# Performance work log

Hardware: AMD Instinct MI355X
Metric: run time of the kernel (lower is better)

## Reference

```python
import jax, jax.numpy as jnp
import numpy as np

N = 100000   # nodes
E = 1200000  # edges
D = 64       # dim == num_features
L = 5        # num_gc_layers
G = 128      # num graphs in batch
BN_EPS = 1e-5
NORM_EPS = 1e-12

def setup_inputs() -> dict:
    key = jax.random.key(0)
    ks = jax.random.split(key, 16)
    s = 0.05
    x = jax.random.normal(ks[0], (N, D), jnp.float32)
    edge_index = jax.random.randint(ks[1], (2, E), 0, N, dtype=jnp.int32)
    batch = jnp.sort(jax.random.randint(ks[2], (N,), 0, G, dtype=jnp.int32))
    # Encoder_support: Linear(D, D)
    Ws = jax.random.normal(ks[3], (D, D), jnp.float32) * s
    bs = jnp.zeros((D,), jnp.float32)
    # GIN MLPs per layer: Linear(D,D) -> ReLU -> Linear(D,D)
    W1 = jax.random.normal(ks[4], (L, D, D), jnp.float32) * s
    b1 = jnp.zeros((L, D), jnp.float32)
    W2 = jax.random.normal(ks[5], (L, D, D), jnp.float32) * s
    b2 = jnp.zeros((L, D), jnp.float32)
    # BatchNorm affine params
    bn_gamma = jnp.ones((L, D), jnp.float32)
    bn_beta = jnp.zeros((L, D), jnp.float32)
    # proj_head: Linear(L*D, L*D) -> ReLU -> Linear(L*D, L*D)
    Wp1 = jax.random.normal(ks[6], (L * D, L * D), jnp.float32) * s
    bp1 = jnp.zeros((L * D,), jnp.float32)
    Wp2 = jax.random.normal(ks[7], (L * D, L * D), jnp.float32) * s
    bp2 = jnp.zeros((L * D,), jnp.float32)
    return {"x": x, "edge_index": edge_index, "batch": batch,
            "Ws": Ws, "bs": bs, "W1": W1, "b1": b1, "W2": W2, "b2": b2,
            "bn_gamma": bn_gamma, "bn_beta": bn_beta,
            "Wp1": Wp1, "bp1": bp1, "Wp2": Wp2, "bp2": bp2}

def _l2norm(v):
    # F.normalize(v, dim=1): v / max(||v||_2, 1e-12)
    n = jnp.sqrt(jnp.sum(v * v, axis=1, keepdims=True))
    return v / jnp.maximum(n, NORM_EPS)

def reference(x, edge_index, batch, Ws, bs, W1, b1, W2, b2,
              bn_gamma, bn_beta, Wp1, bp1, Wp2, bp2):
    src, dst = edge_index[0], edge_index[1]
    h = x @ Ws + bs  # Encoder_support
    xs = []
    for i in range(L):
        # GINConv (eps=0): nn(x + sum_{j->i} x_j)
        agg = jax.ops.segment_sum(h[src], dst, num_segments=N)  # [N, D]
        z = h + agg
        z = jnp.maximum(z @ W1[i] + b1[i], 0.0) @ W2[i] + b2[i]
        z = jnp.maximum(z, 0.0)  # F.relu after conv
        # BatchNorm1d (training-mode batch stats over nodes)
        mean = jnp.mean(z, axis=0)
        var = jnp.var(z, axis=0)
        h = bn_gamma[i] * (z - mean) * jax.lax.rsqrt(var + BN_EPS) + bn_beta[i]
        xs.append(h)
    # global_add_pool per layer, concat along feature dim -> [G, L*D]
    pooled = jnp.concatenate(
        [jax.ops.segment_sum(h_, batch, num_segments=G) for h_ in xs], axis=1)
    y = jnp.maximum(pooled @ Wp1 + bp1, 0.0) @ Wp2 + bp2
    return (_l2norm(y), _l2norm(pooled))
```

## Files before the change

kernel.cpp:

```cpp
#include <hip/hip_runtime.h>
#include <hip/hip_bf16.h>
#include <hip/hip_fp16.h>

constexpr int Nn = 100000;
constexpr int Ee = 1200000;
constexpr int Ll = 5;
constexpr int Gg = 128;
constexpr int PDim = 320;
constexpr int GG = (Nn + 63) / 64;

constexpr int NB    = 98;
constexpr int BCAP  = 16384;
constexpr int CHUNK = 4096;
constexpr int NBLK_A = (Ee + CHUNK - 1) / CHUNK;

typedef float f32x4 __attribute__((ext_vector_type(4)));
typedef _Float16 half8 __attribute__((ext_vector_type(8)));

union U4H8 { uint4 u; half8 h; };

__device__ inline ushort f2h(float f) {
    const __half h = __float2half(f);
    return *(const ushort*)&h;
}
__device__ inline uint pack2h(float lo, float hi) {
    return (uint)f2h(lo) | ((uint)f2h(hi) << 16);
}
__device__ inline float h2f_lo(uint u) {
    const ushort s = (ushort)(u & 0xffffu);
    return __half2float(*(const __half*)&s);
}
__device__ inline float h2f_hi(uint u) {
    const ushort s = (ushort)(u >> 16);
    return __half2float(*(const __half*)&s);
}

__device__ inline int lower_bound_i(const int* __restrict__ a, int n, int v)
{
    int lo = 0, hi = n;
    while (lo < hi) {
        const int m = (lo + hi) >> 1;
        if (a[m] < v) lo = m + 1; else hi = m;
    }
    return lo;
}

__global__ void init_csr(const int* __restrict__ batch, int* __restrict__ gCursor,
                         int* __restrict__ cnt, float* __restrict__ sc)
{
    const int t = threadIdx.x;
    if (t < NB) gCursor[t] = t * BCAP;
    {
        const int lo = lower_bound_i(batch, Nn, t);
        const int hi = lower_bound_i(batch, Nn, t + 1);
        cnt[t] = hi - lo;
    }
    if (t < 64) { sc[t] = 1.f; sc[64 + t] = 0.f; }
}

__global__ __launch_bounds__(256) void conv_weights(
    const float* __restrict__ Ws, const float* __restrict__ W1,
    const float* __restrict__ W2, ushort* __restrict__ WThi,
    ushort* __restrict__ WTlo)
{
    const int m = blockIdx.x;
    const float* src = (m == 0) ? Ws
                     : (m <= 5) ? W1 + (size_t)(m - 1) * 4096
                                : W2 + (size_t)(m - 6) * 4096;
    ushort* dh = WThi + (size_t)m * 4096;
    ushort* dl = WTlo + (size_t)m * 4096;
    const int t = threadIdx.x;
    const int col = t & 63;
    const int k0 = (t >> 6) * 16;
    #pragma unroll
    for (int i = 0; i < 16; i++) {
        const int k = k0 + i;
        const float w = src[k * 64 + col];
        const ushort h = f2h(w);
        dh[col * 64 + k] = h;
        const float resid = (w - h2f_lo((uint)h)) * 2048.0f;
        dl[col * 64 + k] = f2h(resid);
    }
}

__global__ __launch_bounds__(256) void gemm_enc(
    const float* __restrict__ A1,
    const ushort* __restrict__ WThi, const ushort* __restrict__ WTlo,
    const float* __restrict__ bias, ushort* __restrict__ Ys)
{
    const int t = threadIdx.x;
    const int w = t >> 6;
    const int l = t & 63;
    const int lr = l & 15;
    const int lk = l >> 4;

    half8 bHi[4][2], bLo[4][2];
    #pragma unroll
    for (int nt = 0; nt < 4; nt++)
        #pragma unroll
        for (int c = 0; c < 2; c++) {
            const int off = (nt * 16 + lr) * 64 + c * 32 + lk * 8;
            U4H8 uh, ul;
            uh.u = *(const uint4*)(WThi + off);
            ul.u = *(const uint4*)(WTlo + off);
            bHi[nt][c] = uh.h;
            bLo[nt][c] = ul.h;
        }

    const int arow = blockIdx.x * 64 + w * 16 + lr;
    half8 aHi[2], aLo[2];
    if (arow < Nn) {
        #pragma unroll
        for (int c = 0; c < 2; c++) {
            const float* p1 = A1 + (size_t)arow * 64 + c * 32 + lk * 8;
            U4H8 rh, rl;
            #pragma unroll
            for (int i = 0; i < 8; i++) {
                const float xv = p1[i];
                const _Float16 xh = (_Float16)xv;
                rh.h[i] = xh;
                rl.h[i] = (_Float16)((xv - (float)xh) * 2048.0f);
            }
            aHi[c] = rh.h;
            aLo[c] = rl.h;
        }
    } else {
        U4H8 z; z.u = make_uint4(0, 0, 0, 0);
        aHi[0] = aHi[1] = z.h;
        aLo[0] = aLo[1] = z.h;
    }

    f32x4 accH[4] = {}, accL[4] = {};
    #pragma unroll
    for (int nt = 0; nt < 4; nt++)
        #pragma unroll
        for (int c = 0; c < 2; c++) {
            accH[nt] = __builtin_amdgcn_mfma_f32_16x16x32_f16(
                aHi[c], bHi[nt][c], accH[nt], 0, 0, 0);
            accL[nt] = __builtin_amdgcn_mfma_f32_16x16x32_f16(
                aHi[c], bLo[nt][c], accL[nt], 0, 0, 0);
            accL[nt] = __builtin_amdgcn_mfma_f32_16x16x32_f16(
                aLo[c], bHi[nt][c], accL[nt], 0, 0, 0);
        }

    #pragma unroll
    for (int nt = 0; nt < 4; nt++) {
        const int ccol = nt * 16 + lr;
        const float bb = bias[ccol];
        #pragma unroll
        for (int j = 0; j < 4; j++) {
            const int crow = blockIdx.x * 64 + w * 16 + lk * 4 + j;
            if (crow < Nn)
                Ys[(size_t)crow * 64 + ccol] =
                    f2h(fmaf(accL[nt][j], 1.0f / 2048.0f, accH[nt][j]) + bb);
        }
    }
}

__global__ __launch_bounds__(256) void fused_mlp(
    const ushort* __restrict__ Us,
    const ushort* __restrict__ WT1hi, const ushort* __restrict__ WT1lo,
    const float* __restrict__ b1v,
    const ushort* __restrict__ WT2hi, const ushort* __restrict__ WT2lo,
    const float* __restrict__ b2v,
    ushort* __restrict__ Zs, float* __restrict__ spart)
{
    const int t = threadIdx.x;
    const int w = t >> 6;
    const int l = t & 63;
    const int lr = l & 15;
    const int lk = l >> 4;

    __shared__ ushort Mh[64][72];
    __shared__ float red[2][4][4][16];

    half8 b1Hi[4][2], b1Lo[4][2];
    #pragma unroll
    for (int nt = 0; nt < 4; nt++)
        #pragma unroll
        for (int c = 0; c < 2; c++) {
            const int off = (nt * 16 + lr) * 64 + c * 32 + lk * 8;
            U4H8 uh, ul;
            uh.u = *(const uint4*)(WT1hi + off);
            ul.u = *(const uint4*)(WT1lo + off);
            b1Hi[nt][c] = uh.h;
            b1Lo[nt][c] = ul.h;
        }

    const int arow = blockIdx.x * 64 + w * 16 + lr;
    half8 aF[2];
    if (arow < Nn) {
        U4H8 v0, v1;
        v0.u = *(const uint4*)(Us + (size_t)arow * 64 + lk * 8);
        v1.u = *(const uint4*)(Us + (size_t)arow * 64 + 32 + lk * 8);
        aF[0] = v0.h;
        aF[1] = v1.h;
    } else {
        U4H8 z; z.u = make_uint4(0, 0, 0, 0);
        aF[0] = aF[1] = z.h;
    }

    f32x4 accH[4] = {}, accL[4] = {};
    #pragma unroll
    for (int nt = 0; nt < 4; nt++)
        #pragma unroll
        for (int c = 0; c < 2; c++) {
            accH[nt] = __builtin_amdgcn_mfma_f32_16x16x32_f16(
                aF[c], b1Hi[nt][c], accH[nt], 0, 0, 0);
            accL[nt] = __builtin_amdgcn_mfma_f32_16x16x32_f16(
                aF[c], b1Lo[nt][c], accL[nt], 0, 0, 0);
        }

    #pragma unroll
    for (int nt = 0; nt < 4; nt++) {
        const int ccol = nt * 16 + lr;
        const float bb = b1v[ccol];
        #pragma unroll
        for (int j = 0; j < 4; j++) {
            const int rloc = w * 16 + lk * 4 + j;
            const float m = fmaxf(fmaf(accL[nt][j], 1.0f / 2048.0f, accH[nt][j]) + bb, 0.f);
            Mh[rloc][ccol] = f2h(m);
        }
    }
    __syncthreads();

    half8 b2Hi[4][2], b2Lo[4][2];
    #pragma unroll
    for (int nt = 0; nt < 4; nt++)
        #pragma unroll
        for (int c = 0; c < 2; c++) {
            const int off = (nt * 16 + lr) * 64 + c * 32 + lk * 8;
            U4H8 uh, ul;
            uh.u = *(const uint4*)(WT2hi + off);
            ul.u = *(const uint4*)(WT2lo + off);
            b2Hi[nt][c] = uh.h;
            b2Lo[nt][c] = ul.h;
        }

    half8 a2F[2];
    #pragma unroll
    for (int c = 0; c < 2; c++) {
        U4H8 v;
        v.u = *(const uint4*)&Mh[w * 16 + lr][c * 32 + lk * 8];
        a2F[c] = v.h;
    }

    f32x4 acc2H[4] = {}, acc2L[4] = {};
    #pragma unroll
    for (int nt = 0; nt < 4; nt++)
        #pragma unroll
        for (int c = 0; c < 2; c++) {
            acc2H[nt] = __builtin_amdgcn_mfma_f32_16x16x32_f16(
                a2F[c], b2Hi[nt][c], acc2H[nt], 0, 0, 0);
            acc2L[nt] = __builtin_amdgcn_mfma_f32_16x16x32_f16(
                a2F[c], b2Lo[nt][c], acc2L[nt], 0, 0, 0);
        }

    float s[4], s2[4];
    #pragma unroll
    for (int nt = 0; nt < 4; nt++) {
        const int ccol = nt * 16 + lr;
        const float bb = b2v[ccol];
        s[nt] = 0.f; s2[nt] = 0.f;
        #pragma unroll
        for (int j = 0; j < 4; j++) {
            const int crow = blockIdx.x * 64 + w * 16 + lk * 4 + j;
            if (crow < Nn) {
                const float v = fmaxf(fmaf(acc2L[nt][j], 1.0f / 2048.0f, acc2H[nt][j]) + bb, 0.f);
                Zs[(size_t)crow * 64 + ccol] = f2h(v);
                s[nt] += v; s2[nt] += v * v;
            }
        }
    }

    #pragma unroll
    for (int nt = 0; nt < 4; nt++) {
        s[nt]  += __shfl_xor(s[nt], 16);  s[nt]  += __shfl_xor(s[nt], 32);
        s2[nt] += __shfl_xor(s2[nt], 16); s2[nt] += __shfl_xor(s2[nt], 32);
    }
    if (l < 16) {
        #pragma unroll
        for (int nt = 0; nt < 4; nt++) {
            red[0][w][nt][l] = s[nt];
            red[1][w][nt][l] = s2[nt];
        }
    }
    __syncthreads();
    if (t < 64) {
        float ts = 0.f, ts2 = 0.f;
        #pragma unroll
        for (int wv = 0; wv < 4; wv++) {
            ts  += red[0][wv][t >> 4][t & 15];
            ts2 += red[1][wv][t >> 4][t & 15];
        }
        spart[(size_t)blockIdx.x * 128 + t] = ts;
        spart[(size_t)blockIdx.x * 128 + 64 + t] = ts2;
    }
}

__global__ __launch_bounds__(256) void reduce_stats(
    const float* __restrict__ spart, float* __restrict__ stats)
{
    const int t = threadIdx.x;
    const int col = t & 127;
    const int half = t >> 7;
    const int r0 = blockIdx.x * 98;
    const int r1 = min(r0 + 98, GG);
    float acc = 0.f;
    for (int r = r0 + half; r < r1; r += 2)
        acc += spart[(size_t)r * 128 + col];
    atomicAdd(&stats[col], acc);
}

__global__ __launch_bounds__(256) void bin_edges(
    const int* __restrict__ ei, int* __restrict__ gCursor,
    uint2* __restrict__ binned)
{
    __shared__ int hist[NB];
    __shared__ int base[NB];
    __shared__ int cur[NB];
    const int t = threadIdx.x;
    const int e0 = blockIdx.x * CHUNK;
    const int eEnd = min(e0 + CHUNK, Ee);
    if (t < NB) hist[t] = 0;
    __syncthreads();
    for (int e = e0 + t; e < eEnd; e += 256)
        atomicAdd(&hist[ei[Ee + e] >> 10], 1);
    __syncthreads();
    if (t < NB) {
        base[t] = atomicAdd(&gCursor[t], hist[t]);
        cur[t] = 0;
    }
    __syncthreads();
    for (int e = e0 + t; e < eEnd; e += 256) {
        const int s = ei[e];
        const int d = ei[Ee + e];
        const int b = d >> 10;
        const int pos = atomicAdd(&cur[b], 1);
        binned[(size_t)base[b] + pos] = make_uint2((uint)d, (uint)s);
    }
}

__global__ __launch_bounds__(128) void scan_buckets(
    const int* __restrict__ gCursor, int* __restrict__ bucketBase)
{
    __shared__ int sh[128];
    const int t = threadIdx.x;
    const int c = (t < NB) ? gCursor[t] - t * BCAP : 0;
    sh[t] = c;
    __syncthreads();
    for (int off = 1; off < 128; off <<= 1) {
        const int u = (t >= off) ? sh[t - off] : 0;
        __syncthreads();
        sh[t] += u;
        __syncthreads();
    }
    bucketBase[t] = sh[t] - c;
}

__global__ __launch_bounds__(256) void build_csr(
    const uint2* __restrict__ binned, const int* __restrict__ gCursor,
    const int* __restrict__ bucketBase, int* __restrict__ rowptr,
    int* __restrict__ colidx)
{
    __shared__ int degS[1024];
    __shared__ int sh[256];
    __shared__ int colStage[BCAP];
    const int b = blockIdx.x;
    const int t = threadIdx.x;
    const int cnt = gCursor[b] - b * BCAP;
    const int base = bucketBase[b];
    const uint2* src = binned + (size_t)b * BCAP;

    for (int i = t; i < 1024; i += 256) degS[i] = 0;
    __syncthreads();
    for (int i = t; i < cnt; i += 256)
        atomicAdd(&degS[src[i].x & 1023], 1);
    __syncthreads();

    const int b4 = t * 4;
    const int v0 = degS[b4], v1 = degS[b4 + 1], v2 = degS[b4 + 2], v3 = degS[b4 + 3];
    const int sSum = v0 + v1 + v2 + v3;
    sh[t] = sSum;
    __syncthreads();
    for (int off = 1; off < 256; off <<= 1) {
        const int u = (t >= off) ? sh[t - off] : 0;
        __syncthreads();
        sh[t] += u;
        __syncthreads();
    }
    const int excl = sh[t] - sSum;
    const int p0 = excl, p1 = excl + v0, p2 = excl + v0 + v1, p3 = excl + v0 + v1 + v2;

    const int grow = b * 1024 + b4;
    if (grow + 3 <= Nn) {
        *(int4*)(rowptr + grow) = make_int4(base + p0, base + p1, base + p2, base + p3);
    } else {
        if (grow + 0 <= Nn) rowptr[grow + 0] = base + p0;
        if (grow + 1 <= Nn) rowptr[grow + 1] = base + p1;
        if (grow + 2 <= Nn) rowptr[grow + 2] = base + p2;
        if (grow + 3 <= Nn) rowptr[grow + 3] = base + p3;
    }

    degS[b4] = p0; degS[b4 + 1] = p1; degS[b4 + 2] = p2; degS[b4 + 3] = p3;
    __syncthreads();
    for (int i = t; i < cnt; i += 256) {
        const uint2 p = src[i];
        const int pos = atomicAdd(&degS[p.x & 1023], 1);
        colStage[pos] = (int)p.y;
    }
    __syncthreads();
    for (int i = t; i < cnt; i += 256) colidx[base + i] = colStage[i];
}

__global__ __launch_bounds__(256) void gather_bn(
    const int* __restrict__ rowptr, const int* __restrict__ col,
    const ushort* __restrict__ zs, const float* __restrict__ sc,
    ushort* __restrict__ us)
{
    __shared__ float scS[128];
    const int t = threadIdx.x;
    if (t < 128) scS[t] = sc[t];
    __syncthreads();

    const int r = blockIdx.x * 32 + (t >> 3);
    const int q = t & 7;
    const int beg = rowptr[r], end = rowptr[r + 1];
    float a[8];
    {
        const uint4 v = *(const uint4*)(zs + (size_t)r * 64 + q * 8);
        a[0] = h2f_lo(v.x); a[1] = h2f_hi(v.x);
        a[2] = h2f_lo(v.y); a[3] = h2f_hi(v.y);
        a[4] = h2f_lo(v.z); a[5] = h2f_hi(v.z);
        a[6] = h2f_lo(v.w); a[7] = h2f_hi(v.w);
    }
    int j = beg;
    const int end4 = beg + ((end - beg) & ~3);
    for (; j < end4; j += 4) {
        const int s0 = col[j], s1 = col[j + 1], s2 = col[j + 2], s3 = col[j + 3];
        const uint4 v0 = *(const uint4*)(zs + (size_t)s0 * 64 + q * 8);
        const uint4 v1 = *(const uint4*)(zs + (size_t)s1 * 64 + q * 8);
        const uint4 v2 = *(const uint4*)(zs + (size_t)s2 * 64 + q * 8);
        const uint4 v3 = *(const uint4*)(zs + (size_t)s3 * 64 + q * 8);
        a[0] += h2f_lo(v0.x) + h2f_lo(v1.x) + h2f_lo(v2.x) + h2f_lo(v3.x);
        a[1] += h2f_hi(v0.x) + h2f_hi(v1.x) + h2f_hi(v2.x) + h2f_hi(v3.x);
        a[2] += h2f_lo(v0.y) + h2f_lo(v1.y) + h2f_lo(v2.y) + h2f_lo(v3.y);
        a[3] += h2f_hi(v0.y) + h2f_hi(v1.y) + h2f_hi(v2.y) + h2f_hi(v3.y);
        a[4] += h2f_lo(v0.z) + h2f_lo(v1.z) + h2f_lo(v2.z) + h2f_lo(v3.z);
        a[5] += h2f_hi(v0.z) + h2f_hi(v1.z) + h2f_hi(v2.z) + h2f_hi(v3.z);
        a[6] += h2f_lo(v0.w) + h2f_lo(v1.w) + h2f_lo(v2.w) + h2f_lo(v3.w);
        a[7] += h2f_hi(v0.w) + h2f_hi(v1.w) + h2f_hi(v2.w) + h2f_hi(v3.w);
    }
    for (; j < end; j++) {
        const int s = col[j];
        const uint4 v = *(const uint4*)(zs + (size_t)s * 64 + q * 8);
        a[0] += h2f_lo(v.x); a[1] += h2f_hi(v.x);
        a[2] += h2f_lo(v.y); a[3] += h2f_hi(v.y);
        a[4] += h2f_lo(v.z); a[5] += h2f_hi(v.z);
        a[6] += h2f_lo(v.w); a[7] += h2f_hi(v.w);
    }
    const float dgf = (float)(end - beg + 1);
    float o[8];
    #pragma unroll
    for (int i = 0; i < 8; i++)
        o[i] = fmaf(scS[q * 8 + i], a[i], dgf * scS[64 + q * 8 + i]);
    uint4 p;
    p.x = pack2h(o[0], o[1]); p.y = pack2h(o[2], o[3]);
    p.z = pack2h(o[4], o[5]); p.w = pack2h(o[6], o[7]);
    *(uint4*)(us + (size_t)r * 64 + q * 8) = p;
}

__global__ void bn_finalize(
    float* __restrict__ stats, const float* __restrict__ gamma,
    const float* __restrict__ beta, float* __restrict__ sc,
    float* __restrict__ sc5, int layer)
{
    const int c = threadIdx.x;
    const float mean = stats[c] * (1.0f / Nn);
    const float var = stats[64 + c] * (1.0f / Nn) - mean * mean;
    const float scale = gamma[layer * 64 + c] * rsqrtf(var + 1e-5f);
    const float shift = beta[layer * 64 + c] - mean * scale;
    sc[c] = scale;
    sc[64 + c] = shift;
    sc5[layer * 128 + c] = scale;
    sc5[layer * 128 + 64 + c] = shift;
    stats[c] = 0.f;
    stats[64 + c] = 0.f;
}

__global__ __launch_bounds__(256) void pool_z(
    const ushort* __restrict__ zs, const int* __restrict__ batch,
    float* __restrict__ poolZ)
{
    const int g = blockIdx.x >> 3;
    const int sub = blockIdx.x & 7;
    const int lo = lower_bound_i(batch, Nn, g);
    const int hi = lower_bound_i(batch, Nn, g + 1);
    const int t = threadIdx.x;
    const int cq = t & 15;
    const int rg = (t >> 4) + sub * 16;
    float acc[4] = {};
    for (int row = lo + rg; row < hi; row += 128) {
        const uint2 p = *(const uint2*)(zs + (size_t)row * 64 + cq * 4);
        acc[0] += h2f_lo(p.x); acc[1] += h2f_hi(p.x);
        acc[2] += h2f_lo(p.y); acc[3] += h2f_hi(p.y);
    }
    __shared__ float red[16][16][4];
    #pragma unroll
    for (int i = 0; i < 4; i++) red[t >> 4][cq][i] = acc[i];
    __syncthreads();
    if (t < 64) {
        const int c2 = t >> 2, j = t & 3;
        float s = 0.f;
        #pragma unroll
        for (int r = 0; r < 16; r++) s += red[r][c2][j];
        atomicAdd(&poolZ[g * 64 + c2 * 4 + j], s);
    }
}

__global__ __launch_bounds__(256) void final_pool(
    const float* __restrict__ sc5, const float* __restrict__ poolZ,
    const int* __restrict__ cnt, float* __restrict__ pooled)
{
    const int idx = blockIdx.x * 256 + threadIdx.x;
    const int c = idx & 63;
    const int g = (idx >> 6) & 127;
    const int l = idx >> 13;
    pooled[g * PDim + l * 64 + c] =
        sc5[l * 128 + c] * poolZ[(size_t)l * Gg * 64 + g * 64 + c]
        + (float)cnt[g] * sc5[l * 128 + 64 + c];
}

template<bool RELU>
__global__ __launch_bounds__(256) void proj(
    const float* __restrict__ X, const float* __restrict__ W,
    const float* __restrict__ bias, float* __restrict__ Y)
{
    const int idx = blockIdx.x * 256 + threadIdx.x;
    const int r = idx / PDim;
    const int c = idx - r * PDim;
    float acc = bias[c];
    #pragma unroll 8
    for (int k = 0; k < PDim; k++)
        acc = fmaf(X[r * PDim + k], W[k * PDim + c], acc);
    if constexpr (RELU) acc = fmaxf(acc, 0.f);
    Y[idx] = acc;
}

__global__ __launch_bounds__(64) void l2norm_rows(
    const float* __restrict__ X, float* __restrict__ out)
{
    const int r = blockIdx.x;
    const int l = threadIdx.x;
    float v[5];
    float s = 0.f;
    #pragma unroll
    for (int i = 0; i < 5; i++) {
        v[i] = X[r * PDim + i * 64 + l];
        s += v[i] * v[i];
    }
    #pragma unroll
    for (int off = 32; off > 0; off >>= 1) s += __shfl_down(s, off);
    s = __shfl(s, 0);
    const float d = fmaxf(sqrtf(s), 1e-12f);
    #pragma unroll
    for (int i = 0; i < 5; i++)
        out[r * PDim + i * 64 + l] = v[i] / d;
}

extern "C" void kernel_launch(void* const* d_in, const int* in_sizes, int n_in,
                              void* d_out, int out_size, void* d_ws, size_t ws_size,
                              hipStream_t stream)
{
    const float* x     = (const float*)d_in[0];
    const int*   ei    = (const int*)d_in[1];
    const int*   batch = (const int*)d_in[2];
    const float* Ws    = (const float*)d_in[3];
    const float* bs    = (const float*)d_in[4];
    const float* W1    = (const float*)d_in[5];
    const float* b1    = (const float*)d_in[6];
    const float* W2    = (const float*)d_in[7];
    const float* b2    = (const float*)d_in[8];
    const float* gamma = (const float*)d_in[9];
    const float* beta  = (const float*)d_in[10];
    const float* Wp1   = (const float*)d_in[11];
    const float* bp1   = (const float*)d_in[12];
    const float* Wp2   = (const float*)d_in[13];
    const float* bp2   = (const float*)d_in[14];
    float* out = (float*)d_out;

    ushort* Us = (ushort*)d_ws;
    ushort* Zs = Us + (size_t)Nn * 64;
    ushort* WThi = Zs + (size_t)Nn * 64;
    ushort* WTlo = WThi + 11 * 4096;
    float* pooled = (float*)(WTlo + 11 * 4096);
    float* ytmp   = pooled + (size_t)Gg * PDim;
    float* ypro   = ytmp + (size_t)Gg * PDim;
    float* stats  = ypro + (size_t)Gg * PDim;
    float* sc     = stats + 128;
    float* sc5    = sc + 128;
    float* poolZ  = sc5 + 5 * 128;
    float* spart  = poolZ + 5 * Gg * 64;
    int* cnt    = (int*)(spart + (size_t)GG * 128);
    int* rowptr = cnt + 128;
    int* colidx = rowptr + Nn + 1;
    int* gCursor = colidx + Ee;
    int* bucketBase = gCursor + 128;
    size_t woff = (size_t)((bucketBase + 128) - (int*)d_ws);
    woff = (woff + 1) & ~(size_t)1;
    uint2* binned = (uint2*)((int*)d_ws + woff);

    hipMemsetAsync(stats, 0, 128 * sizeof(float), stream);
    hipMemsetAsync(poolZ, 0, 5 * Gg * 64 * sizeof(float), stream);

    init_csr<<<1, 128, 0, stream>>>(batch, gCursor, cnt, sc);
    conv_weights<<<11, 256, 0, stream>>>(Ws, W1, W2, WThi, WTlo);

    bin_edges<<<NBLK_A, 256, 0, stream>>>(ei, gCursor, binned);
    scan_buckets<<<1, 128, 0, stream>>>(gCursor, bucketBase);
    build_csr<<<NB, 256, 0, stream>>>(binned, gCursor, bucketBase, rowptr, colidx);

    gemm_enc<<<GG, 256, 0, stream>>>(x, WThi, WTlo, bs, Zs);

    for (int l = 0; l < Ll; l++) {
        gather_bn<<<Nn / 32, 256, 0, stream>>>(rowptr, colidx, Zs, sc, Us);
        fused_mlp<<<GG, 256, 0, stream>>>(
            Us,
            WThi + (size_t)(1 + l) * 4096, WTlo + (size_t)(1 + l) * 4096,
            b1 + (size_t)l * 64,
            WThi + (size_t)(6 + l) * 4096, WTlo + (size_t)(6 + l) * 4096,
            b2 + (size_t)l * 64,
            Zs, spart);
        reduce_stats<<<16, 256, 0, stream>>>(spart, stats);
        bn_finalize<<<1, 64, 0, stream>>>(stats, gamma, beta, sc, sc5, l);
        pool_z<<<Gg * 8, 256, 0, stream>>>(Zs, batch, poolZ + (size_t)l * Gg * 64);
    }

    final_pool<<<160, 256, 0, stream>>>(sc5, poolZ, cnt, pooled);

    proj<true><<<160, 256, 0, stream>>>(pooled, Wp1, bp1, ytmp);
    proj<false><<<160, 256, 0, stream>>>(ytmp, Wp2, bp2, ypro);

    l2norm_rows<<<Gg, 64, 0, stream>>>(ypro, out);
    l2norm_rows<<<Gg, 64, 0, stream>>>(pooled, out + Gg * PDim);
}
```

Before: 570.6 us.

## Reuse per-block column sums for graph pooling and drop stats atomics

New measurement: 774.2 us. 1.36x slower.

```diff
diff --git a/kernel.cpp b/kernel.cpp
--- a/kernel.cpp
+++ b/kernel.cpp
@@ -34,6 +34,9 @@
     const ushort s = (ushort)(u >> 16);
     return __half2float(*(const __half*)&s);
 }
+__device__ inline float h2f(ushort s) {
+    return __half2float(*(const __half*)&s);
+}
 
 __device__ inline int lower_bound_i(const int* __restrict__ a, int n, int v)
 {
@@ -78,7 +81,7 @@
         const float w = src[k * 64 + col];
         const ushort h = f2h(w);
         dh[col * 64 + k] = h;
-        const float resid = (w - h2f_lo((uint)h)) * 2048.0f;
+        const float resid = (w - h2f(h)) * 2048.0f;
         dl[col * 64 + k] = f2h(resid);
     }
 }
@@ -298,18 +301,63 @@
     }
 }
 
-__global__ __launch_bounds__(256) void reduce_stats(
-    const float* __restrict__ spart, float* __restrict__ stats)
-{
-    const int t = threadIdx.x;
-    const int col = t & 127;
-    const int half = t >> 7;
+__global__ __launch_bounds__(128) void reduce_stats(
+    const float* __restrict__ spart, float* __restrict__ sp16)
+{
+    const int t = threadIdx.x;
     const int r0 = blockIdx.x * 98;
     const int r1 = min(r0 + 98, GG);
     float acc = 0.f;
-    for (int r = r0 + half; r < r1; r += 2)
-        acc += spart[(size_t)r * 128 + col];
-    atomicAdd(&stats[col], acc);
+    for (int r = r0; r < r1; r++)
+        acc += spart[(size_t)r * 128 + t];
+    sp16[(size_t)blockIdx.x * 128 + t] = acc;
+}
+
+__global__ void bn_finalize(
+    const float* __restrict__ sp16, const float* __restrict__ gamma,
+    const float* __restrict__ beta, float* __restrict__ sc,
+    float* __restrict__ sc5, int layer)
+{
+    const int c = threadIdx.x;
+    float sum = 0.f, sum2 = 0.f;
+    #pragma unroll
+    for (int b = 0; b < 16; b++) {
+        sum  += sp16[b * 128 + c];
+        sum2 += sp16[b * 128 + 64 + c];
+    }
+    const float mean = sum * (1.0f / Nn);
+    const float var = sum2 * (1.0f / Nn) - mean * mean;
+    const float scale = gamma[layer * 64 + c] * rsqrtf(var + 1e-5f);
+    const float shift = beta[layer * 64 + c] - mean * scale;
+    sc[c] = scale;
+    sc[64 + c] = shift;
+    sc5[layer * 128 + c] = scale;
+    sc5[layer * 128 + 64 + c] = shift;
+}
+
+__global__ __launch_bounds__(64) void reduce_pool(
+    const float* __restrict__ spart, const ushort* __restrict__ zs,
+    const int* __restrict__ batch, float* __restrict__ poolZ)
+{
+    const int g = blockIdx.x;
+    const int c = threadIdx.x;
+    const int lo = lower_bound_i(batch, Nn, g);
+    const int hi = lower_bound_i(batch, Nn, g + 1);
+    const int bs = (lo + 63) >> 6;
+    const int be = hi >> 6;
+    float acc = 0.f;
+    if (bs <= be) {
+        for (int b = bs; b < be; b++)
+            acc += spart[(size_t)b * 128 + c];
+        for (int r = lo; r < bs * 64; r++)
+            acc += h2f(zs[(size_t)r * 64 + c]);
+        for (int r = be * 64; r < hi; r++)
+            acc += h2f(zs[(size_t)r * 64 + c]);
+    } else {
+        for (int r = lo; r < hi; r++)
+            acc += h2f(zs[(size_t)r * 64 + c]);
+    }
+    poolZ[g * 64 + c] = acc;
 }
 
 __global__ __launch_bounds__(256) void bin_edges(
@@ -435,21 +483,21 @@
         a[6] = h2f_lo(v.w); a[7] = h2f_hi(v.w);
     }
     int j = beg;
-    const int end4 = beg + ((end - beg) & ~3);
-    for (; j < end4; j += 4) {
-        const int s0 = col[j], s1 = col[j + 1], s2 = col[j + 2], s3 = col[j + 3];
-        const uint4 v0 = *(const uint4*)(zs + (size_t)s0 * 64 + q * 8);
-        const uint4 v1 = *(const uint4*)(zs + (size_t)s1 * 64 + q * 8);
-        const uint4 v2 = *(const uint4*)(zs + (size_t)s2 * 64 + q * 8);
-        const uint4 v3 = *(const uint4*)(zs + (size_t)s3 * 64 + q * 8);
-        a[0] += h2f_lo(v0.x) + h2f_lo(v1.x) + h2f_lo(v2.x) + h2f_lo(v3.x);
-        a[1] += h2f_hi(v0.x) + h2f_hi(v1.x) + h2f_hi(v2.x) + h2f_hi(v3.x);
-        a[2] += h2f_lo(v0.y) + h2f_lo(v1.y) + h2f_lo(v2.y) + h2f_lo(v3.y);
-        a[3] += h2f_hi(v0.y) + h2f_hi(v1.y) + h2f_hi(v2.y) + h2f_hi(v3.y);
-        a[4] += h2f_lo(v0.z) + h2f_lo(v1.z) + h2f_lo(v2.z) + h2f_lo(v3.z);
-        a[5] += h2f_hi(v0.z) + h2f_hi(v1.z) + h2f_hi(v2.z) + h2f_hi(v3.z);
-        a[6] += h2f_lo(v0.w) + h2f_lo(v1.w) + h2f_lo(v2.w) + h2f_lo(v3.w);
-        a[7] += h2f_hi(v0.w) + h2f_hi(v1.w) + h2f_hi(v2.w) + h2f_hi(v3.w);
+    const int end8 = beg + ((end - beg) & ~7);
+    for (; j < end8; j += 8) {
+        uint4 v[8];
+        #pragma unroll
+        for (int k = 0; k < 8; k++) {
+            const int s = col[j + k];
+            v[k] = *(const uint4*)(zs + (size_t)s * 64 + q * 8);
+        }
+        #pragma unroll
+        for (int k = 0; k < 8; k++) {
+            a[0] += h2f_lo(v[k].x); a[1] += h2f_hi(v[k].x);
+            a[2] += h2f_lo(v[k].y); a[3] += h2f_hi(v[k].y);
+            a[4] += h2f_lo(v[k].z); a[5] += h2f_hi(v[k].z);
+            a[6] += h2f_lo(v[k].w); a[7] += h2f_hi(v[k].w);
+        }
     }
     for (; j < end; j++) {
         const int s = col[j];
@@ -468,54 +516,6 @@
     p.x = pack2h(o[0], o[1]); p.y = pack2h(o[2], o[3]);
     p.z = pack2h(o[4], o[5]); p.w = pack2h(o[6], o[7]);
     *(uint4*)(us + (size_t)r * 64 + q * 8) = p;
-}
-
-__global__ void bn_finalize(
-    float* __restrict__ stats, const float* __restrict__ gamma,
-    const float* __restrict__ beta, float* __restrict__ sc,
-    float* __restrict__ sc5, int layer)
-{
-    const int c = threadIdx.x;
-    const float mean = stats[c] * (1.0f / Nn);
-    const float var = stats[64 + c] * (1.0f / Nn) - mean * mean;
-    const float scale = gamma[layer * 64 + c] * rsqrtf(var + 1e-5f);
-    const float shift = beta[layer * 64 + c] - mean * scale;
-    sc[c] = scale;
-    sc[64 + c] = shift;
-    sc5[layer * 128 + c] = scale;
-    sc5[layer * 128 + 64 + c] = shift;
-    stats[c] = 0.f;
-    stats[64 + c] = 0.f;
-}
-
-__global__ __launch_bounds__(256) void pool_z(
-    const ushort* __restrict__ zs, const int* __restrict__ batch,
-    float* __restrict__ poolZ)
-{
-    const int g = blockIdx.x >> 3;
-    const int sub = blockIdx.x & 7;
-    const int lo = lower_bound_i(batch, Nn, g);
-    const int hi = lower_bound_i(batch, Nn, g + 1);
-    const int t = threadIdx.x;
-    const int cq = t & 15;
-    const int rg = (t >> 4) + sub * 16;
-    float acc[4] = {};
-    for (int row = lo + rg; row < hi; row += 128) {
-        const uint2 p = *(const uint2*)(zs + (size_t)row * 64 + cq * 4);
-        acc[0] += h2f_lo(p.x); acc[1] += h2f_hi(p.x);
-        acc[2] += h2f_lo(p.y); acc[3] += h2f_hi(p.y);
-    }
-    __shared__ float red[16][16][4];
-    #pragma unroll
-    for (int i = 0; i < 4; i++) red[t >> 4][cq][i] = acc[i];
-    __syncthreads();
-    if (t < 64) {
-        const int c2 = t >> 2, j = t & 3;
-        float s = 0.f;
-        #pragma unroll
-        for (int r = 0; r < 16; r++) s += red[r][c2][j];
-        atomicAdd(&poolZ[g * 64 + c2 * 4 + j], s);
-    }
 }
 
 __global__ __launch_bounds__(256) void final_pool(
@@ -596,8 +596,8 @@
     float* pooled = (float*)(WTlo + 11 * 4096);
     float* ytmp   = pooled + (size_t)Gg * PDim;
     float* ypro   = ytmp + (size_t)Gg * PDim;
-    float* stats  = ypro + (size_t)Gg * PDim;
-    float* sc     = stats + 128;
+    float* sp16   = ypro + (size_t)Gg * PDim;
+    float* sc     = sp16 + 16 * 128;
     float* sc5    = sc + 128;
     float* poolZ  = sc5 + 5 * 128;
     float* spart  = poolZ + 5 * Gg * 64;
@@ -610,9 +610,6 @@
     woff = (woff + 1) & ~(size_t)1;
     uint2* binned = (uint2*)((int*)d_ws + woff);
 
-    hipMemsetAsync(stats, 0, 128 * sizeof(float), stream);
-    hipMemsetAsync(poolZ, 0, 5 * Gg * 64 * sizeof(float), stream);
-
     init_csr<<<1, 128, 0, stream>>>(batch, gCursor, cnt, sc);
     conv_weights<<<11, 256, 0, stream>>>(Ws, W1, W2, WThi, WTlo);
 
@@ -631,9 +628,10 @@
             WThi + (size_t)(6 + l) * 4096, WTlo + (size_t)(6 + l) * 4096,
             b2 + (size_t)l * 64,
             Zs, spart);
-        reduce_stats<<<16, 256, 0, stream>>>(spart, stats);
-        bn_finalize<<<1, 64, 0, stream>>>(stats, gamma, beta, sc, sc5, l);
-        pool_z<<<Gg * 8, 256, 0, stream>>>(Zs, batch, poolZ + (size_t)l * Gg * 64);
+        reduce_stats<<<16, 128, 0, stream>>>(spart, sp16);
+        bn_finalize<<<1, 64, 0, stream>>>(sp16, gamma, beta, sc, sc5, l);
+        reduce_pool<<<Gg, 64, 0, stream>>>(spart, Zs, batch,
+                                           poolZ + (size_t)l * Gg * 64);
     }
 
     final_pool<<<160, 256, 0, stream>>>(sc5, poolZ, cnt, pooled);
```
